# Performance work log

Hardware: AMD Instinct MI355X
Metric: run time of the kernel (lower is better)

Reference implementation:

```python
import jax, jax.numpy as jnp
import numpy as np

INPUT_DIM = 1024
OUTPUT_DIM = 1024
DEGREE = 8
N_TOKENS = 8192


def setup_inputs() -> dict:
    key = jax.random.key(0)
    k1, k2 = jax.random.split(key)
    x = jax.random.normal(k1, (N_TOKENS, INPUT_DIM), dtype=jnp.float32)
    # xavier_normal_ with gain = 1/(input_dim*(degree+1)) over fan dims (output_dim, degree+1)
    fan_in, fan_out = OUTPUT_DIM, DEGREE + 1  # torch treats dim0/dim1 as fans; scale is tiny anyway
    gain = 1.0 / (INPUT_DIM * (DEGREE + 1))
    std = gain * np.sqrt(2.0 / (INPUT_DIM + OUTPUT_DIM))
    cheby_coeffs = std * jax.random.normal(k2, (INPUT_DIM, OUTPUT_DIM, DEGREE + 1), dtype=jnp.float32)
    return {"x": x, "cheby_coeffs": cheby_coeffs}


def reference(x, cheby_coeffs):
    # x: (..., input_dim) -> y: (..., output_dim)
    degree_p1 = cheby_coeffs.shape[-1]
    theta = jnp.arccos(jnp.tanh(x))                      # (..., i)
    arange = jnp.arange(degree_p1, dtype=x.dtype)        # (d,)
    basis = jnp.cos(theta[..., None] * arange)           # (..., i, d) Chebyshev T_d(tanh(x))
    y = jnp.einsum('...id,iod->...o', basis, cheby_coeffs)
    return y
```

## Files before the change

### kernel.cpp

```cpp
#include <hip/hip_runtime.h>


typedef __bf16 bf16;
typedef __bf16 bf16x8 __attribute__((ext_vector_type(8)));
typedef float f32x4 __attribute__((ext_vector_type(4)));

#define KSTAGES 128

__device__ __forceinline__ void g2lds16(const void* g, void* l) {
  __builtin_amdgcn_global_load_lds(
      (const __attribute__((address_space(1))) unsigned int*)g,
      (__attribute__((address_space(3))) unsigned int*)l, 16, 0, 0);
}

__global__ __launch_bounds__(256)
void cheby_prep(const float* __restrict__ C, bf16* __restrict__ Bt,
                float* __restrict__ bias) {
  __shared__ float tile[32][289];
  const int it = blockIdx.x, i0 = it * 32, o0 = blockIdx.y * 32;
  const int tid = threadIdx.x;
  for (int idx = tid; idx < 32 * 288; idx += 256) {
    int i = idx / 288, c = idx - i * 288;
    tile[i][c] = C[(size_t)(i0 + i) * 9216 + (size_t)o0 * 9 + c];
  }
  __syncthreads();
  for (int idx = tid; idx < 1024; idx += 256) {
    int o  = idx >> 5;
    int p  = (idx >> 3) & 3;
    int cp = idx & 7;
    int og = o0 + o;
    int c  = cp ^ (og & 7);
    int d  = 2 * p + 1 + (c >> 2);
    int ib = (c & 3) * 8;
    bf16x8 v;
    #pragma unroll
    for (int e = 0; e < 8; ++e) v[e] = (bf16)tile[ib + e][o * 9 + d];
    *(bf16x8*)&Bt[((size_t)og * KSTAGES + it * 4 + p) * 64 + cp * 8] = v;
  }
  if (tid < 32) {
    float s = 0.f;
    #pragma unroll
    for (int i = 0; i < 32; ++i) s += tile[i][tid * 9];
    atomicAdd(&bias[o0 + tid], s);
  }
}

__global__ __launch_bounds__(512, 4)
void cheby_gemm(const float* __restrict__ x, const bf16* __restrict__ Bt,
                const float* __restrict__ bias, float* __restrict__ out) {
  __shared__ bf16 As[128 * 64];
  __shared__ bf16 Bs[128 * 64];

  const int tid  = threadIdx.x;
  const int lane = tid & 63, w = tid >> 6;
  const int wm = w >> 2, wn = w & 3;
  const int mb = blockIdx.x >> 3, nb = blockIdx.x & 7;
  const int t0 = mb * 128, o0 = nb * 128;

  const int arow = tid >> 2, q = tid & 3;
  const int aw0 = arow * 64 + ((q ^ (arow & 7)) * 8);
  const int aw1 = arow * 64 + (((q + 4) ^ (arow & 7)) * 8);
  const float* xp = x + (size_t)(t0 + arow) * 1024 + q * 8;

  const int brow = w * 16 + (lane >> 3);
  const size_t bg0 = (size_t)(o0 + brow) * (KSTAGES * 64) + (size_t)(lane & 7) * 8;
  const size_t bg1 = (size_t)(o0 + brow + 8) * (KSTAGES * 64) + (size_t)(lane & 7) * 8;
  bf16* bl0 = &Bs[w * 1024];
  bf16* bl1 = &Bs[w * 1024 + 512];

  const int ml = lane & 15, kc = lane >> 4;

  f32x4 acc[4][2];
  #pragma unroll
  for (int a = 0; a < 4; ++a)
    #pragma unroll
    for (int b = 0; b < 2; ++b) acc[a][b] = (f32x4){0.f, 0.f, 0.f, 0.f};

  f32x4 xv0 = *(const f32x4*)(xp);
  f32x4 xv1 = *(const f32x4*)(xp + 4);

  #pragma unroll 1
  for (int it = 0; it < 32; ++it) {
    float t2[8], cur[8], prev[8];
    {
      float xs[8] = {xv0.x, xv0.y, xv0.z, xv0.w, xv1.x, xv1.y, xv1.z, xv1.w};
      #pragma unroll
      for (int j = 0; j < 8; ++j) {
        float e  = __expf(xs[j] + xs[j]);
        float th = 1.f - 2.f / (e + 1.f);
        t2[j] = th + th;
        cur[j] = th; prev[j] = 1.f;
      }
    }
    #pragma unroll 1
    for (int p = 0; p < 4; ++p) {
      __syncthreads();
      bf16x8 pk0, pk1;
      #pragma unroll
      for (int j = 0; j < 8; ++j) {
        pk0[j] = (bf16)cur[j];
        float nx = __builtin_fmaf(t2[j], cur[j], -prev[j]);
        prev[j] = cur[j]; cur[j] = nx;
      }
      #pragma unroll
      for (int j = 0; j < 8; ++j) {
        pk1[j] = (bf16)cur[j];
        float nx = __builtin_fmaf(t2[j], cur[j], -prev[j]);
        prev[j] = cur[j]; cur[j] = nx;
      }
      *(bf16x8*)&As[aw0] = pk0;
      *(bf16x8*)&As[aw1] = pk1;
      {
        const size_t soff = (size_t)(it * 4 + p) * 64;
        g2lds16(Bt + bg0 + soff, bl0);
        g2lds16(Bt + bg1 + soff, bl1);
      }
      if (p == 0 && it < 31) {
        xv0 = *(const f32x4*)(xp + (it + 1) * 32);
        xv1 = *(const f32x4*)(xp + (it + 1) * 32 + 4);
      }
      __syncthreads();
      #pragma unroll
      for (int ks = 0; ks < 2; ++ks) {
        const int cp = ((ks * 4 + kc) ^ (ml & 7)) * 8;
        bf16x8 af[4], bfr[2];
        #pragma unroll
        for (int mt = 0; mt < 4; ++mt)
          af[mt] = *(const bf16x8*)&As[(wm * 64 + mt * 16 + ml) * 64 + cp];
        #pragma unroll
        for (int nt = 0; nt < 2; ++nt)
          bfr[nt] = *(const bf16x8*)&Bs[(wn * 32 + nt * 16 + ml) * 64 + cp];
        #pragma unroll
        for (int mt = 0; mt < 4; ++mt)
          #pragma unroll
          for (int nt = 0; nt < 2; ++nt)
            acc[mt][nt] = __builtin_amdgcn_mfma_f32_16x16x32_bf16(af[mt], bfr[nt], acc[mt][nt], 0, 0, 0);
      }
    }
  }

  const int quad = lane >> 4;
  const int obase = o0 + wn * 32 + ml;
  const size_t rbase = (size_t)(t0 + wm * 64 + quad * 4) * 1024;
  float bv0 = bias[obase], bv1 = bias[obase + 16];
  #pragma unroll
  for (int mt = 0; mt < 4; ++mt)
    #pragma unroll
    for (int r = 0; r < 4; ++r) {
      out[rbase + (size_t)(mt * 16 + r) * 1024 + obase]      = acc[mt][0][r] + bv0;
      out[rbase + (size_t)(mt * 16 + r) * 1024 + obase + 16] = acc[mt][1][r] + bv1;
    }
}

__global__ __launch_bounds__(256)
void cheby_naive(const float* __restrict__ x, const float* __restrict__ C,
                 float* __restrict__ out) {
  const int t = blockIdx.x, tid = threadIdx.x;
  float acc[4] = {0.f, 0.f, 0.f, 0.f};
  for (int i = 0; i < 1024; ++i) {
    float th = tanhf(x[(size_t)t * 1024 + i]);
    float T[9]; T[0] = 1.f; T[1] = th;
    #pragma unroll
    for (int d = 2; d < 9; ++d) T[d] = 2.f * th * T[d - 1] - T[d - 2];
    #pragma unroll
    for (int j = 0; j < 4; ++j) {
      const float* cp = &C[((size_t)i * 1024 + tid + j * 256) * 9];
      float s = 0.f;
      #pragma unroll
      for (int d = 0; d < 9; ++d) s += T[d] * cp[d];
      acc[j] += s;
    }
  }
  #pragma unroll
  for (int j = 0; j < 4; ++j) out[(size_t)t * 1024 + tid + j * 256] = acc[j];
}

extern "C" void kernel_launch(void* const* d_in, const int* in_sizes, int n_in,
                              void* d_out, int out_size, void* d_ws, size_t ws_size,
                              hipStream_t stream) {
  (void)in_sizes; (void)n_in; (void)out_size;
  const float* x = (const float*)d_in[0];
  const float* C = (const float*)d_in[1];
  float* out = (float*)d_out;

  const size_t bt_bytes = (size_t)1024 * KSTAGES * 64 * sizeof(bf16);
  if (ws_size >= bt_bytes + 1024 * sizeof(float)) {
    bf16*  Bt   = (bf16*)d_ws;
    float* bias = (float*)((char*)d_ws + bt_bytes);
    hipMemsetAsync(bias, 0, 1024 * sizeof(float), stream);
    cheby_prep<<<dim3(32, 32), 256, 0, stream>>>(C, Bt, bias);
    cheby_gemm<<<512, 512, 0, stream>>>(x, Bt, bias, out);
  } else {
    cheby_naive<<<8192, 256, 0, stream>>>(x, C, out);
  }
}
```

Before: 282.3 us.

## Double-buffer LDS stages and widen GEMM tile to 128x256

The GEMM kernel now uses double-buffered LDS for both the Chebyshev basis tile and the coefficient tile. The next stage is generated and loaded while the current stage's MFMAs run, and each stage needs one barrier instead of two. The output tile widens from 128x128 to 128x256, so each wave holds 4x4 accumulators and loads of the generated A operand are reused across more columns. The grid halves to 256 blocks and the occupancy hint drops to 2 blocks per CU, which trades parallelism and register pressure for more reuse.

```diff
diff --git a/kernel.cpp b/kernel.cpp
--- a/kernel.cpp
+++ b/kernel.cpp
@@ -45,44 +45,40 @@
   }
 }
 
-__global__ __launch_bounds__(512, 4)
+__global__ __launch_bounds__(512, 2)
 void cheby_gemm(const float* __restrict__ x, const bf16* __restrict__ Bt,
                 const float* __restrict__ bias, float* __restrict__ out) {
-  __shared__ bf16 As[128 * 64];
-  __shared__ bf16 Bs[128 * 64];
+  __shared__ bf16 As[2][128 * 64];
+  __shared__ bf16 Bs[2][256 * 64];
 
   const int tid  = threadIdx.x;
   const int lane = tid & 63, w = tid >> 6;
   const int wm = w >> 2, wn = w & 3;
-  const int mb = blockIdx.x >> 3, nb = blockIdx.x & 7;
-  const int t0 = mb * 128, o0 = nb * 128;
+  const int nb = blockIdx.x & 3, mb = blockIdx.x >> 2;
+  const int t0 = mb * 128, o0 = nb * 256;
 
   const int arow = tid >> 2, q = tid & 3;
   const int aw0 = arow * 64 + ((q ^ (arow & 7)) * 8);
   const int aw1 = arow * 64 + (((q + 4) ^ (arow & 7)) * 8);
   const float* xp = x + (size_t)(t0 + arow) * 1024 + q * 8;
 
-  const int brow = w * 16 + (lane >> 3);
-  const size_t bg0 = (size_t)(o0 + brow) * (KSTAGES * 64) + (size_t)(lane & 7) * 8;
-  const size_t bg1 = (size_t)(o0 + brow + 8) * (KSTAGES * 64) + (size_t)(lane & 7) * 8;
-  bf16* bl0 = &Bs[w * 1024];
-  bf16* bl1 = &Bs[w * 1024 + 512];
+  const size_t bg = (size_t)(o0 + w * 32 + (lane >> 3)) * (KSTAGES * 64) + (size_t)(lane & 7) * 8;
 
-  const int ml = lane & 15, kc = lane >> 4;
+  const int ml = lane & 15, kc = lane >> 4, ml7 = lane & 7;
 
-  f32x4 acc[4][2];
+  f32x4 acc[4][4];
   #pragma unroll
   for (int a = 0; a < 4; ++a)
     #pragma unroll
-    for (int b = 0; b < 2; ++b) acc[a][b] = (f32x4){0.f, 0.f, 0.f, 0.f};
+    for (int b = 0; b < 4; ++b) acc[a][b] = (f32x4){0.f, 0.f, 0.f, 0.f};
 
   f32x4 xv0 = *(const f32x4*)(xp);
   f32x4 xv1 = *(const f32x4*)(xp + 4);
+  float t2[8], cur[8], prev[8];
 
-  #pragma unroll 1
-  for (int it = 0; it < 32; ++it) {
-    float t2[8], cur[8], prev[8];
-    {
+  auto gen = [&](int k) {
+    const int bi = k & 1;
+    if ((k & 3) == 0) {
       float xs[8] = {xv0.x, xv0.y, xv0.z, xv0.w, xv1.x, xv1.y, xv1.z, xv1.w};
       #pragma unroll
       for (int j = 0; j < 8; ++j) {
@@ -91,65 +87,72 @@
         t2[j] = th + th;
         cur[j] = th; prev[j] = 1.f;
       }
+      const int itn = (k >> 2) + 1;
+      if (itn < 32) {
+        xv0 = *(const f32x4*)(xp + itn * 32);
+        xv1 = *(const f32x4*)(xp + itn * 32 + 4);
+      }
     }
-    #pragma unroll 1
-    for (int p = 0; p < 4; ++p) {
-      __syncthreads();
-      bf16x8 pk0, pk1;
+    bf16x8 pk0, pk1;
+    #pragma unroll
+    for (int j = 0; j < 8; ++j) {
+      pk0[j] = (bf16)cur[j];
+      float nx = __builtin_fmaf(t2[j], cur[j], -prev[j]);
+      prev[j] = cur[j]; cur[j] = nx;
+    }
+    #pragma unroll
+    for (int j = 0; j < 8; ++j) {
+      pk1[j] = (bf16)cur[j];
+      float nx = __builtin_fmaf(t2[j], cur[j], -prev[j]);
+      prev[j] = cur[j]; cur[j] = nx;
+    }
+    *(bf16x8*)&As[bi][aw0] = pk0;
+    *(bf16x8*)&As[bi][aw1] = pk1;
+    const size_t soff = (size_t)k * 64;
+    #pragma unroll
+    for (int b = 0; b < 4; ++b)
+      g2lds16(Bt + bg + (size_t)b * 8 * (KSTAGES * 64) + soff,
+              &Bs[bi][(w * 32 + b * 8) * 64]);
+  };
+
+  gen(0);
+
+  #pragma unroll 1
+  for (int s = 0; s < KSTAGES; ++s) {
+    const int bi = s & 1;
+    __syncthreads();
+    if (s < KSTAGES - 1) gen(s + 1);
+    #pragma unroll
+    for (int ks = 0; ks < 2; ++ks) {
+      const int cp = ((ks * 4 + kc) ^ ml7) * 8;
+      bf16x8 af[4], bfr[4];
       #pragma unroll
-      for (int j = 0; j < 8; ++j) {
-        pk0[j] = (bf16)cur[j];
-        float nx = __builtin_fmaf(t2[j], cur[j], -prev[j]);
-        prev[j] = cur[j]; cur[j] = nx;
-      }
+      for (int mt = 0; mt < 4; ++mt)
+        af[mt] = *(const bf16x8*)&As[bi][(wm * 64 + mt * 16 + ml) * 64 + cp];
       #pragma unroll
-      for (int j = 0; j < 8; ++j) {
-        pk1[j] = (bf16)cur[j];
-        float nx = __builtin_fmaf(t2[j], cur[j], -prev[j]);
-        prev[j] = cur[j]; cur[j] = nx;
-      }
-      *(bf16x8*)&As[aw0] = pk0;
-      *(bf16x8*)&As[aw1] = pk1;
-      {
-        const size_t soff = (size_t)(it * 4 + p) * 64;
-        g2lds16(Bt + bg0 + soff, bl0);
-        g2lds16(Bt + bg1 + soff, bl1);
-      }
-      if (p == 0 && it < 31) {
-        xv0 = *(const f32x4*)(xp + (it + 1) * 32);
-        xv1 = *(const f32x4*)(xp + (it + 1) * 32 + 4);
-      }
-      __syncthreads();
+      for (int nt = 0; nt < 4; ++nt)
+        bfr[nt] = *(const bf16x8*)&Bs[bi][(wn * 64 + nt * 16 + ml) * 64 + cp];
       #pragma unroll
-      for (int ks = 0; ks < 2; ++ks) {
-        const int cp = ((ks * 4 + kc) ^ (ml & 7)) * 8;
-        bf16x8 af[4], bfr[2];
+      for (int mt = 0; mt < 4; ++mt)
         #pragma unroll
-        for (int mt = 0; mt < 4; ++mt)
-          af[mt] = *(const bf16x8*)&As[(wm * 64 + mt * 16 + ml) * 64 + cp];
-        #pragma unroll
-        for (int nt = 0; nt < 2; ++nt)
-          bfr[nt] = *(const bf16x8*)&Bs[(wn * 32 + nt * 16 + ml) * 64 + cp];
-        #pragma unroll
-        for (int mt = 0; mt < 4; ++mt)
-          #pragma unroll
-          for (int nt = 0; nt < 2; ++nt)
-            acc[mt][nt] = __builtin_amdgcn_mfma_f32_16x16x32_bf16(af[mt], bfr[nt], acc[mt][nt], 0, 0, 0);
-      }
+        for (int nt = 0; nt < 4; ++nt)
+          acc[mt][nt] = __builtin_amdgcn_mfma_f32_16x16x32_bf16(af[mt], bfr[nt], acc[mt][nt], 0, 0, 0);
     }
   }
 
   const int quad = lane >> 4;
-  const int obase = o0 + wn * 32 + ml;
+  const int obase = o0 + wn * 64 + ml;
   const size_t rbase = (size_t)(t0 + wm * 64 + quad * 4) * 1024;
-  float bv0 = bias[obase], bv1 = bias[obase + 16];
+  float bv[4];
+  #pragma unroll
+  for (int nt = 0; nt < 4; ++nt) bv[nt] = bias[obase + nt * 16];
   #pragma unroll
   for (int mt = 0; mt < 4; ++mt)
     #pragma unroll
-    for (int r = 0; r < 4; ++r) {
-      out[rbase + (size_t)(mt * 16 + r) * 1024 + obase]      = acc[mt][0][r] + bv0;
-      out[rbase + (size_t)(mt * 16 + r) * 1024 + obase + 16] = acc[mt][1][r] + bv1;
-    }
+    for (int r = 0; r < 4; ++r)
+      #pragma unroll
+      for (int nt = 0; nt < 4; ++nt)
+        out[rbase + (size_t)(mt * 16 + r) * 1024 + obase + nt * 16] = acc[mt][nt][r] + bv[nt];
 }
 
 __global__ __launch_bounds__(256)
@@ -189,7 +192,7 @@
     float* bias = (float*)((char*)d_ws + bt_bytes);
     hipMemsetAsync(bias, 0, 1024 * sizeof(float), stream);
     cheby_prep<<<dim3(32, 32), 256, 0, stream>>>(C, Bt, bias);
-    cheby_gemm<<<512, 512, 0, stream>>>(x, Bt, bias, out);
+    cheby_gemm<<<256, 512, 0, stream>>>(x, Bt, bias, out);
   } else {
     cheby_naive<<<8192, 256, 0, stream>>>(x, C, out);
   }
```

Result: faster. 269.8 us (-4.4%).
